# Performance work log

Measured on AMD Instinct MI355X. Metric: run time of the kernel, lower is better.

## Reference

```python
import jax, jax.numpy as jnp
import numpy as np

NUM_BITS = 8  # byte_size default used by HilbertFlatten.forward -> hilbert_flatten(x)


def _hilbert_flat_indices(shape, num_bits=NUM_BITS):
    """Flat (raveled) source index for each position along the Hilbert curve.

    Vectorized Skilling-style decode, matching numpy-hilbert-curve's decode():
    hilbert ints 0..N-1 -> D-dim coords, then ravel to flat gather indices.
    Data-independent: depends only on the array shape.
    """
    num_dims = len(shape)
    n = int(np.prod(shape))
    nb_total = num_dims * num_bits
    s = np.arange(n, dtype=np.uint64)
    # Unpack bits MSB-first: (n, num_dims*num_bits). Done column-wise to avoid a
    # huge uint64 intermediate.
    bits = np.empty((n, nb_total), dtype=bool)
    for j in range(nb_total):
        shift = np.uint64(nb_total - 1 - j)
        bits[:, j] = (s >> shift) & np.uint64(1)
    # binary -> gray:  g = h ^ (h >> 1)
    gray = bits.copy()
    gray[:, 1:] ^= bits[:, :-1]
    # De-interleave: (n, num_bits, num_dims) -> (n, num_dims, num_bits)
    gray = np.swapaxes(gray.reshape(n, num_bits, num_dims), 1, 2).copy()
    # Undo the encode transforms: iterate backwards through bits and dims.
    for bit in range(num_bits - 1, -1, -1):
        for dim in range(num_dims - 1, -1, -1):
            mask = gray[:, dim, bit][:, None]
            # Where bit is on: invert dim-0 lower bits.
            gray[:, 0, bit + 1:] ^= mask
            # Where bit is off: swap lower bits of dim with dim 0.
            to_flip = ~mask & (gray[:, 0, bit + 1:] ^ gray[:, dim, bit + 1:])
            gray[:, dim, bit + 1:] ^= to_flip
            gray[:, 0, bit + 1:] ^= to_flip
    # Pack bit-planes back to integer coordinates: (n, num_dims)
    pows = (1 << np.arange(num_bits - 1, -1, -1)).astype(np.int64)
    locs = (gray.astype(np.int64) * pows).sum(-1)
    return np.ravel_multi_index(tuple(locs.T), shape)


def setup_inputs() -> dict:
    key = jax.random.key(0)
    x = jax.random.normal(key, (256, 256, 256), dtype=jnp.float32)
    return {"x": x}


def reference(x):
    # hilbert_flatten: out[s] = x[decode(s)] for s in 0..N-1  ->  1-D array of N
    perm = jnp.asarray(_hilbert_flat_indices(tuple(x.shape)))
    return jnp.take(x.reshape(-1), perm)
```

## Files before the change

kernel.cpp:

```cpp
#include <hip/hip_runtime.h>


typedef float f32x4 __attribute__((ext_vector_type(4)));
typedef __attribute__((address_space(1))) const void global_cvoid;
typedef __attribute__((address_space(3))) void lds_void;

__device__ __forceinline__ void decode8(unsigned S, unsigned B[3],
                                        unsigned& baseflat) {
    unsigned g = S ^ (S >> 1);
    unsigned G[3];
#pragma unroll
    for (int d = 0; d < 3; ++d) {
        unsigned v = (g >> (2 - d)) & 0x00249249u;
        v = (v ^ (v >> 2)) & 0x030C30C3u;
        v = (v ^ (v >> 4)) & 0x0300F00Fu;
        v = (v ^ (v >> 8)) & 0x000000FFu;
        G[d] = v;
    }
    G[0] |= 0x100u; G[1] |= 0x200u; G[2] |= 0x400u;
#pragma unroll
    for (int bit = 6; bit >= 0; --bit) {
        const unsigned low = ((1u << (7 - bit)) - 1u) | 0x0F00u;
#pragma unroll
        for (int dim = 2; dim >= 0; --dim) {
            unsigned m = (G[dim] >> (7 - bit)) & 1u;
            unsigned diff = (G[0] ^ G[dim]) & low;
            unsigned t = diff & (m - 1u);
            G[0] ^= ((0u - m) & low) ^ t;
            G[dim] ^= t;
        }
    }
    unsigned s3m = 0u - ((S >> 3) & 1u);
    unsigned V0 = (0xF0u ^ s3m) & 0xFFu;
    const unsigned V1 = 0x3Cu, V2 = 0x66u;
#pragma unroll
    for (int d = 0; d < 3; ++d) {
        unsigned cd = 0u - ((G[d] >> 11) & 1u);
        unsigned a0 = (0u - ((G[d] >> 8) & 1u)) ^ cd;
        unsigned a1 = (0u - ((G[d] >> 9) & 1u)) ^ cd;
        unsigned a2 = (0u - ((G[d] >> 10) & 1u)) ^ cd;
        B[d] = ((a0 & V0) ^ (a1 & V1) ^ (a2 & V2) ^ cd) & 0xFFu;
    }
    baseflat = ((G[0] & 0xFEu) << 16) | ((G[1] & 0xFEu) << 8) | (G[2] & 0xFEu);
}

__global__ __launch_bounds__(256) void hilbert_r2_kernel(
    const float* __restrict__ x, float* __restrict__ out) {
    __shared__ float lds[4 * 1024];
    unsigned nb = blockIdx.x;
    unsigned cpx = gridDim.x >> 3;
    unsigned b = (nb & 7u) * cpx + (nb >> 3);
    unsigned tid = threadIdx.x;
    unsigned lane = tid & 63u;
    unsigned wave = tid >> 6;
    unsigned W = b * 4u + wave;
    unsigned Sw = W * 1024u;

    unsigned B0[3], B1[3], bf0, bf1;
    decode8(Sw + lane * 8u, B0, bf0);
    decode8(Sw + 512u + lane * 8u, B1, bf1);

    unsigned dxl = lane >> 4;
    unsigned dyl = (lane >> 1) & 7u;
    unsigned half = lane & 1u;
    auto lds3 = (__attribute__((address_space(3))) float*)lds;
    unsigned rf0 = bf0 & 0x00F8F8F8u;
    unsigned rf1 = bf1 & 0x00F8F8F8u;
#pragma unroll
    for (unsigned q = 0; q < 2; ++q) {
        const float* gbase = x + (q ? rf1 : rf0);
#pragma unroll
        for (unsigned h = 0; h < 2; ++h) {
            const float* src = gbase + (h * 4u + dxl) * 65536u
                             + dyl * 256u + half * 4u;
            __builtin_amdgcn_global_load_lds(
                (global_cvoid*)src,
                (lds_void*)(lds3 + wave * 1024u + q * 512u + h * 256u),
                16, 0, 0);
        }
    }
    asm volatile("s_waitcnt vmcnt(0)" ::: "memory");

#pragma unroll
    for (unsigned q = 0; q < 2; ++q) {
        unsigned baseflat = q ? bf1 : bf0;
        const unsigned* B = q ? B1 : B0;
        unsigned bx = (baseflat >> 16) & 6u;
        unsigned by = (baseflat >> 8) & 6u;
        unsigned bz = baseflat & 6u;
        unsigned bxp = (bx >> 1) & 1u;
        unsigned byp = (by >> 1) & 1u;
        const float* lw = lds + wave * 1024u + q * 512u;
        float2 r0 = *(const float2*)&lw[(bx + byp) * 64u + (by + bxp) * 8u + bz];
        float2 r1 = *(const float2*)&lw[(bx + byp) * 64u + (by + (bxp ^ 1u)) * 8u + bz];
        float2 r2 = *(const float2*)&lw[(bx + (byp ^ 1u)) * 64u + (by + bxp) * 8u + bz];
        float2 r3 = *(const float2*)&lw[(bx + (byp ^ 1u)) * 64u + (by + (bxp ^ 1u)) * 8u + bz];
        bool sx = bxp != 0u, sy = byp != 0u;
        float2 a0 = sx ? r1 : r0;
        float2 a1 = sx ? r0 : r1;
        float2 a2 = sx ? r3 : r2;
        float2 a3 = sx ? r2 : r3;
        float2 q00 = sy ? a2 : a0;
        float2 q01 = sy ? a3 : a1;
        float2 q10 = sy ? a0 : a2;
        float2 q11 = sy ? a1 : a3;

        float o8[8];
#pragma unroll
        for (int rr = 0; rr < 8; ++rr) {
            unsigned f0 = (B[0] >> rr) & 1u;
            unsigned f1 = (B[1] >> rr) & 1u;
            unsigned f2 = (B[2] >> rr) & 1u;
            float2 t0 = f1 ? q01 : q00;
            float2 t1 = f1 ? q11 : q10;
            float2 t  = f0 ? t1 : t0;
            o8[rr] = f2 ? t.y : t.x;
        }

        int src1 = (int)(lane >> 1);
        int src2 = (int)(32u + (lane >> 1));
        bool hi = (lane & 1u) != 0u;
        float vA[4], vB[4];
#pragma unroll
        for (int j = 0; j < 4; ++j) {
            float a = __shfl(o8[j], src1, 64);
            float bb = __shfl(o8[4 + j], src1, 64);
            vA[j] = hi ? bb : a;
            float c = __shfl(o8[j], src2, 64);
            float d = __shfl(o8[4 + j], src2, 64);
            vB[j] = hi ? d : c;
        }
        unsigned WB = Sw + q * 512u;
        __builtin_nontemporal_store((f32x4){vA[0], vA[1], vA[2], vA[3]},
                                    (f32x4*)(out + WB + 4u * lane));
        __builtin_nontemporal_store((f32x4){vB[0], vB[1], vB[2], vB[3]},
                                    (f32x4*)(out + WB + 256u + 4u * lane));
    }
}

extern "C" void kernel_launch(void* const* d_in, const int* in_sizes, int n_in,
                              void* d_out, int out_size, void* d_ws, size_t ws_size,
                              hipStream_t stream) {
    const float* x = (const float*)d_in[0];
    float* out = (float*)d_out;
    unsigned n = (unsigned)out_size;
    unsigned nwaves = n / 1024u;
    unsigned blocks = nwaves / 4u;
    hilbert_r2_kernel<<<blocks, 256, 0, stream>>>(x, out);
}
```

Before: 26.61 us.

## Double-buffer per-wave Hilbert chunks so gathers overlap with shuffle and store

Each wave now handles four 512-element chunks instead of two, and the grid is halved to match. Two LDS halves are reused as a double buffer. The next chunk's decode and async global-to-LDS load are issued while the previous chunk is permuted and stored, with explicit vmcnt waits counting both outstanding loads and stores. The goal is to hide gather latency behind compute and stores, at the cost of fewer blocks in flight and hand-tuned wait counts that must stay in step with the instruction order.

```diff
diff --git a/kernel.cpp b/kernel.cpp
--- a/kernel.cpp
+++ b/kernel.cpp
@@ -4,6 +4,7 @@
 typedef float f32x4 __attribute__((ext_vector_type(4)));
 typedef __attribute__((address_space(1))) const void global_cvoid;
 typedef __attribute__((address_space(3))) void lds_void;
+typedef __attribute__((address_space(3))) float lds_float;
 
 __device__ __forceinline__ void decode8(unsigned S, unsigned B[3],
                                         unsigned& baseflat) {
@@ -44,7 +45,77 @@
     baseflat = ((G[0] & 0xFEu) << 16) | ((G[1] & 0xFEu) << 8) | (G[2] & 0xFEu);
 }
 
-__global__ __launch_bounds__(256) void hilbert_r2_kernel(
+__device__ __forceinline__ void issue_loads(const float* __restrict__ x,
+                                            unsigned rf, lds_float* dst,
+                                            unsigned lane) {
+    unsigned dxl = lane >> 4;
+    unsigned dyl = (lane >> 1) & 7u;
+    unsigned half = lane & 1u;
+    const float* gb = x + rf;
+#pragma unroll
+    for (unsigned h = 0; h < 2; ++h) {
+        const float* src = gb + (h * 4u + dxl) * 65536u + dyl * 256u + half * 4u;
+        __builtin_amdgcn_global_load_lds((global_cvoid*)src,
+                                         (lds_void*)(dst + h * 256u), 16, 0, 0);
+    }
+}
+
+__device__ __forceinline__ void process_store(const float* lw,
+                                              const unsigned B[3],
+                                              unsigned baseflat,
+                                              float* __restrict__ outp,
+                                              unsigned lane) {
+    unsigned bx = (baseflat >> 16) & 6u;
+    unsigned by = (baseflat >> 8) & 6u;
+    unsigned bz = baseflat & 6u;
+    unsigned bxp = (bx >> 1) & 1u;
+    unsigned byp = (by >> 1) & 1u;
+    float2 r0 = *(const float2*)&lw[(bx + byp) * 64u + (by + bxp) * 8u + bz];
+    float2 r1 = *(const float2*)&lw[(bx + byp) * 64u + (by + (bxp ^ 1u)) * 8u + bz];
+    float2 r2 = *(const float2*)&lw[(bx + (byp ^ 1u)) * 64u + (by + bxp) * 8u + bz];
+    float2 r3 = *(const float2*)&lw[(bx + (byp ^ 1u)) * 64u + (by + (bxp ^ 1u)) * 8u + bz];
+    bool sx = bxp != 0u, sy = byp != 0u;
+    float2 a0 = sx ? r1 : r0;
+    float2 a1 = sx ? r0 : r1;
+    float2 a2 = sx ? r3 : r2;
+    float2 a3 = sx ? r2 : r3;
+    float2 q00 = sy ? a2 : a0;
+    float2 q01 = sy ? a3 : a1;
+    float2 q10 = sy ? a0 : a2;
+    float2 q11 = sy ? a1 : a3;
+
+    float o8[8];
+#pragma unroll
+    for (int rr = 0; rr < 8; ++rr) {
+        unsigned f0 = (B[0] >> rr) & 1u;
+        unsigned f1 = (B[1] >> rr) & 1u;
+        unsigned f2 = (B[2] >> rr) & 1u;
+        float2 t0 = f1 ? q01 : q00;
+        float2 t1 = f1 ? q11 : q10;
+        float2 t  = f0 ? t1 : t0;
+        o8[rr] = f2 ? t.y : t.x;
+    }
+
+    int src1 = (int)(lane >> 1);
+    int src2 = (int)(32u + (lane >> 1));
+    bool hi = (lane & 1u) != 0u;
+    float vA[4], vB[4];
+#pragma unroll
+    for (int j = 0; j < 4; ++j) {
+        float a = __shfl(o8[j], src1, 64);
+        float bb = __shfl(o8[4 + j], src1, 64);
+        vA[j] = hi ? bb : a;
+        float c = __shfl(o8[j], src2, 64);
+        float d = __shfl(o8[4 + j], src2, 64);
+        vB[j] = hi ? d : c;
+    }
+    __builtin_nontemporal_store((f32x4){vA[0], vA[1], vA[2], vA[3]},
+                                (f32x4*)(outp + 4u * lane));
+    __builtin_nontemporal_store((f32x4){vB[0], vB[1], vB[2], vB[3]},
+                                (f32x4*)(outp + 256u + 4u * lane));
+}
+
+__global__ __launch_bounds__(256) void hilbert_pipe_kernel(
     const float* __restrict__ x, float* __restrict__ out) {
     __shared__ float lds[4 * 1024];
     unsigned nb = blockIdx.x;
@@ -54,88 +125,33 @@
     unsigned lane = tid & 63u;
     unsigned wave = tid >> 6;
     unsigned W = b * 4u + wave;
-    unsigned Sw = W * 1024u;
+    unsigned Sw = W * 2048u;
 
-    unsigned B0[3], B1[3], bf0, bf1;
+    const float* lw = lds + wave * 1024u;
+    lds_float* lw3 = (lds_float*)lds + wave * 1024u;
+
+    unsigned B0[3], B1[3], B2[3], B3[3], bf0, bf1, bf2, bf3;
+
     decode8(Sw + lane * 8u, B0, bf0);
+    issue_loads(x, bf0 & 0x00F8F8F8u, lw3, lane);
     decode8(Sw + 512u + lane * 8u, B1, bf1);
+    issue_loads(x, bf1 & 0x00F8F8F8u, lw3 + 512u, lane);
 
-    unsigned dxl = lane >> 4;
-    unsigned dyl = (lane >> 1) & 7u;
-    unsigned half = lane & 1u;
-    auto lds3 = (__attribute__((address_space(3))) float*)lds;
-    unsigned rf0 = bf0 & 0x00F8F8F8u;
-    unsigned rf1 = bf1 & 0x00F8F8F8u;
-#pragma unroll
-    for (unsigned q = 0; q < 2; ++q) {
-        const float* gbase = x + (q ? rf1 : rf0);
-#pragma unroll
-        for (unsigned h = 0; h < 2; ++h) {
-            const float* src = gbase + (h * 4u + dxl) * 65536u
-                             + dyl * 256u + half * 4u;
-            __builtin_amdgcn_global_load_lds(
-                (global_cvoid*)src,
-                (lds_void*)(lds3 + wave * 1024u + q * 512u + h * 256u),
-                16, 0, 0);
-        }
-    }
-    asm volatile("s_waitcnt vmcnt(0)" ::: "memory");
+    asm volatile("s_waitcnt vmcnt(2)" ::: "memory");
+    process_store(lw, B0, bf0, out + Sw, lane);
+    decode8(Sw + 1024u + lane * 8u, B2, bf2);
+    issue_loads(x, bf2 & 0x00F8F8F8u, lw3, lane);
 
-#pragma unroll
-    for (unsigned q = 0; q < 2; ++q) {
-        unsigned baseflat = q ? bf1 : bf0;
-        const unsigned* B = q ? B1 : B0;
-        unsigned bx = (baseflat >> 16) & 6u;
-        unsigned by = (baseflat >> 8) & 6u;
-        unsigned bz = baseflat & 6u;
-        unsigned bxp = (bx >> 1) & 1u;
-        unsigned byp = (by >> 1) & 1u;
-        const float* lw = lds + wave * 1024u + q * 512u;
-        float2 r0 = *(const float2*)&lw[(bx + byp) * 64u + (by + bxp) * 8u + bz];
-        float2 r1 = *(const float2*)&lw[(bx + byp) * 64u + (by + (bxp ^ 1u)) * 8u + bz];
-        float2 r2 = *(const float2*)&lw[(bx + (byp ^ 1u)) * 64u + (by + bxp) * 8u + bz];
-        float2 r3 = *(const float2*)&lw[(bx + (byp ^ 1u)) * 64u + (by + (bxp ^ 1u)) * 8u + bz];
-        bool sx = bxp != 0u, sy = byp != 0u;
-        float2 a0 = sx ? r1 : r0;
-        float2 a1 = sx ? r0 : r1;
-        float2 a2 = sx ? r3 : r2;
-        float2 a3 = sx ? r2 : r3;
-        float2 q00 = sy ? a2 : a0;
-        float2 q01 = sy ? a3 : a1;
-        float2 q10 = sy ? a0 : a2;
-        float2 q11 = sy ? a1 : a3;
+    asm volatile("s_waitcnt vmcnt(4)" ::: "memory");
+    process_store(lw + 512u, B1, bf1, out + Sw + 512u, lane);
+    decode8(Sw + 1536u + lane * 8u, B3, bf3);
+    issue_loads(x, bf3 & 0x00F8F8F8u, lw3 + 512u, lane);
 
-        float o8[8];
-#pragma unroll
-        for (int rr = 0; rr < 8; ++rr) {
-            unsigned f0 = (B[0] >> rr) & 1u;
-            unsigned f1 = (B[1] >> rr) & 1u;
-            unsigned f2 = (B[2] >> rr) & 1u;
-            float2 t0 = f1 ? q01 : q00;
-            float2 t1 = f1 ? q11 : q10;
-            float2 t  = f0 ? t1 : t0;
-            o8[rr] = f2 ? t.y : t.x;
-        }
+    asm volatile("s_waitcnt vmcnt(4)" ::: "memory");
+    process_store(lw, B2, bf2, out + Sw + 1024u, lane);
 
-        int src1 = (int)(lane >> 1);
-        int src2 = (int)(32u + (lane >> 1));
-        bool hi = (lane & 1u) != 0u;
-        float vA[4], vB[4];
-#pragma unroll
-        for (int j = 0; j < 4; ++j) {
-            float a = __shfl(o8[j], src1, 64);
-            float bb = __shfl(o8[4 + j], src1, 64);
-            vA[j] = hi ? bb : a;
-            float c = __shfl(o8[j], src2, 64);
-            float d = __shfl(o8[4 + j], src2, 64);
-            vB[j] = hi ? d : c;
-        }
-        unsigned WB = Sw + q * 512u;
-        __builtin_nontemporal_store((f32x4){vA[0], vA[1], vA[2], vA[3]},
-                                    (f32x4*)(out + WB + 4u * lane));
-        __builtin_nontemporal_store((f32x4){vB[0], vB[1], vB[2], vB[3]},
-                                    (f32x4*)(out + WB + 256u + 4u * lane));
-    }
+    asm volatile("s_waitcnt vmcnt(2)" ::: "memory");
+    process_store(lw + 512u, B3, bf3, out + Sw + 1536u, lane);
 }
 
 extern "C" void kernel_launch(void* const* d_in, const int* in_sizes, int n_in,
@@ -144,7 +160,7 @@
     const float* x = (const float*)d_in[0];
     float* out = (float*)d_out;
     unsigned n = (unsigned)out_size;
-    unsigned nwaves = n / 1024u;
+    unsigned nwaves = n / 2048u;
     unsigned blocks = nwaves / 4u;
-    hilbert_r2_kernel<<<blocks, 256, 0, stream>>>(x, out);
+    hilbert_pipe_kernel<<<blocks, 256, 0, stream>>>(x, out);
 }
```

Result: slower. 32.64 us (+22.7%).

## Load one 16^3 Hilbert block per workgroup into shared LDS with XOR swizzle

Applied to the files above, without the earlier changes.

Each workgroup now covers 4096 consecutive Hilbert indices, which form one 16x16x16 cube. The four waves cooperatively load the whole cube into LDS as 16-row slabs with an XOR swizzle, instead of each wave loading its own two 8x8x8 sub-cubes. A block-wide barrier follows the loads, and the second decode is moved between issuing the loads and waiting on them to hide latency. Each global load now reads contiguous 64-byte row segments, which improves coalescing and reduces bank conflicts, at the cost of a __syncthreads and swizzle address arithmetic.

```diff
diff --git a/kernel.cpp b/kernel.cpp
--- a/kernel.cpp
+++ b/kernel.cpp
@@ -4,6 +4,7 @@
 typedef float f32x4 __attribute__((ext_vector_type(4)));
 typedef __attribute__((address_space(1))) const void global_cvoid;
 typedef __attribute__((address_space(3))) void lds_void;
+typedef __attribute__((address_space(3))) float lds_float;
 
 __device__ __forceinline__ void decode8(unsigned S, unsigned B[3],
                                         unsigned& baseflat) {
@@ -44,57 +45,62 @@
     baseflat = ((G[0] & 0xFEu) << 16) | ((G[1] & 0xFEu) << 8) | (G[2] & 0xFEu);
 }
 
-__global__ __launch_bounds__(256) void hilbert_r2_kernel(
+__device__ __forceinline__ float2 lds_read2(const float* lds, unsigned ix,
+                                            unsigned iy, unsigned iz) {
+    unsigned c = ix * 64u + iy * 4u + (iz >> 2);
+    unsigned k = ((ix >> 1) & 3u) ^ ((iy >> 1) & 3u);
+    unsigned w = ((c ^ k) << 2) | (iz & 3u);
+    return *(const float2*)&lds[w];
+}
+
+__global__ __launch_bounds__(256) void hilbert_blk_kernel(
     const float* __restrict__ x, float* __restrict__ out) {
-    __shared__ float lds[4 * 1024];
+    __shared__ float lds[4096];
     unsigned nb = blockIdx.x;
     unsigned cpx = gridDim.x >> 3;
     unsigned b = (nb & 7u) * cpx + (nb >> 3);
     unsigned tid = threadIdx.x;
     unsigned lane = tid & 63u;
     unsigned wave = tid >> 6;
-    unsigned W = b * 4u + wave;
-    unsigned Sw = W * 1024u;
+    unsigned Sreg = b << 12;
 
     unsigned B0[3], B1[3], bf0, bf1;
-    decode8(Sw + lane * 8u, B0, bf0);
-    decode8(Sw + 512u + lane * 8u, B1, bf1);
+    decode8(Sreg + wave * 1024u + lane * 8u, B0, bf0);
 
-    unsigned dxl = lane >> 4;
-    unsigned dyl = (lane >> 1) & 7u;
-    unsigned half = lane & 1u;
-    auto lds3 = (__attribute__((address_space(3))) float*)lds;
-    unsigned rf0 = bf0 & 0x00F8F8F8u;
-    unsigned rf1 = bf1 & 0x00F8F8F8u;
+    unsigned X0 = (bf0 >> 16) & 0xF0u;
+    unsigned Y0 = (bf0 >> 8) & 0xF0u;
+    unsigned Z0 = bf0 & 0xF0u;
+    const float* gb = x + (X0 * 65536u + Y0 * 256u + Z0);
+    lds_float* lp = (lds_float*)lds;
+    unsigned j = lane >> 2;
+    unsigned qn = lane & 3u;
 #pragma unroll
-    for (unsigned q = 0; q < 2; ++q) {
-        const float* gbase = x + (q ? rf1 : rf0);
-#pragma unroll
-        for (unsigned h = 0; h < 2; ++h) {
-            const float* src = gbase + (h * 4u + dxl) * 65536u
-                             + dyl * 256u + half * 4u;
-            __builtin_amdgcn_global_load_lds(
-                (global_cvoid*)src,
-                (lds_void*)(lds3 + wave * 1024u + q * 512u + h * 256u),
-                16, 0, 0);
-        }
+    for (unsigned h = 0; h < 4; ++h) {
+        unsigned i = wave * 4u + h;
+        unsigned k = ((i >> 1) & 3u) ^ ((j >> 1) & 3u);
+        unsigned qs = qn ^ k;
+        const float* src = gb + i * 65536u + j * 256u + qs * 4u;
+        __builtin_amdgcn_global_load_lds((global_cvoid*)src,
+                                         (lds_void*)(lp + i * 256u + lane * 4u),
+                                         16, 0, 0);
     }
+    decode8(Sreg + wave * 1024u + 512u + lane * 8u, B1, bf1);
     asm volatile("s_waitcnt vmcnt(0)" ::: "memory");
+    __syncthreads();
 
 #pragma unroll
     for (unsigned q = 0; q < 2; ++q) {
-        unsigned baseflat = q ? bf1 : bf0;
+        unsigned bf = q ? bf1 : bf0;
         const unsigned* B = q ? B1 : B0;
-        unsigned bx = (baseflat >> 16) & 6u;
-        unsigned by = (baseflat >> 8) & 6u;
-        unsigned bz = baseflat & 6u;
-        unsigned bxp = (bx >> 1) & 1u;
-        unsigned byp = (by >> 1) & 1u;
-        const float* lw = lds + wave * 1024u + q * 512u;
-        float2 r0 = *(const float2*)&lw[(bx + byp) * 64u + (by + bxp) * 8u + bz];
-        float2 r1 = *(const float2*)&lw[(bx + byp) * 64u + (by + (bxp ^ 1u)) * 8u + bz];
-        float2 r2 = *(const float2*)&lw[(bx + (byp ^ 1u)) * 64u + (by + bxp) * 8u + bz];
-        float2 r3 = *(const float2*)&lw[(bx + (byp ^ 1u)) * 64u + (by + (bxp ^ 1u)) * 8u + bz];
+        unsigned lx = (bf >> 16) & 14u;
+        unsigned ly = (bf >> 8) & 14u;
+        unsigned lz = bf & 14u;
+        unsigned bxp = (lx >> 1) & 1u;
+        unsigned byp = (ly >> 1) & 1u;
+        float2 r0 = lds_read2(lds, lx + byp,        ly + bxp,        lz);
+        float2 r1 = lds_read2(lds, lx + byp,        ly + (bxp ^ 1u), lz);
+        float2 r2 = lds_read2(lds, lx + (byp ^ 1u), ly + bxp,        lz);
+        float2 r3 = lds_read2(lds, lx + (byp ^ 1u), ly + (bxp ^ 1u), lz);
         bool sx = bxp != 0u, sy = byp != 0u;
         float2 a0 = sx ? r1 : r0;
         float2 a1 = sx ? r0 : r1;
@@ -122,15 +128,15 @@
         bool hi = (lane & 1u) != 0u;
         float vA[4], vB[4];
 #pragma unroll
-        for (int j = 0; j < 4; ++j) {
-            float a = __shfl(o8[j], src1, 64);
-            float bb = __shfl(o8[4 + j], src1, 64);
-            vA[j] = hi ? bb : a;
-            float c = __shfl(o8[j], src2, 64);
-            float d = __shfl(o8[4 + j], src2, 64);
-            vB[j] = hi ? d : c;
+        for (int jj = 0; jj < 4; ++jj) {
+            float a = __shfl(o8[jj], src1, 64);
+            float bb = __shfl(o8[4 + jj], src1, 64);
+            vA[jj] = hi ? bb : a;
+            float c = __shfl(o8[jj], src2, 64);
+            float d = __shfl(o8[4 + jj], src2, 64);
+            vB[jj] = hi ? d : c;
         }
-        unsigned WB = Sw + q * 512u;
+        unsigned WB = Sreg + wave * 1024u + q * 512u;
         __builtin_nontemporal_store((f32x4){vA[0], vA[1], vA[2], vA[3]},
                                     (f32x4*)(out + WB + 4u * lane));
         __builtin_nontemporal_store((f32x4){vB[0], vB[1], vB[2], vB[3]},
@@ -144,7 +150,6 @@
     const float* x = (const float*)d_in[0];
     float* out = (float*)d_out;
     unsigned n = (unsigned)out_size;
-    unsigned nwaves = n / 1024u;
-    unsigned blocks = nwaves / 4u;
-    hilbert_r2_kernel<<<blocks, 256, 0, stream>>>(x, out);
+    unsigned blocks = n >> 12;
+    hilbert_blk_kernel<<<blocks, 256, 0, stream>>>(x, out);
 }
```

Result: slower. 27.40 us (+3.0%).
